# Optimization experiments

Measured on AMD Instinct MI355X. Metric: run time of the kernel, lower is better.

The kernel has to match this reference:

```python
import jax, jax.numpy as jnp
import numpy as np

N, E, IN, HID, Z, H = 10000, 320000, 128, 128, 64, 4


def setup_inputs() -> dict:
    key = jax.random.key(0)
    ks = jax.random.split(key, 24)
    s = 0.05
    inp = {
        "x": jax.random.normal(ks[0], (N, IN), jnp.float32),
        "edge_index": jax.random.randint(ks[1], (2, E), 0, N, jnp.int32),
        "eps": jax.random.normal(ks[2], (N, Z), jnp.float32),
        # GCNConv params
        "gcn_w": jax.random.normal(ks[3], (IN, HID), jnp.float32) * s,
        "gcn_b": jnp.zeros((HID,), jnp.float32),
        # GATConv params (heads=H, out=HID per head, concat=False)
        "gat_w": jax.random.normal(ks[4], (HID, H * HID), jnp.float32) * s,
        "gat_att_src": jax.random.normal(ks[5], (H, HID), jnp.float32) * s,
        "gat_att_dst": jax.random.normal(ks[6], (H, HID), jnp.float32) * s,
        "gat_b": jnp.zeros((HID,), jnp.float32),
        # encoder MLP
        "mlp_w1": jax.random.normal(ks[7], (HID, HID), jnp.float32) * s,
        "mlp_b1": jnp.zeros((HID,), jnp.float32),
        "mlp_w2": jax.random.normal(ks[8], (HID, HID), jnp.float32) * s,
        "mlp_b2": jnp.zeros((HID,), jnp.float32),
        "mu_w": jax.random.normal(ks[9], (HID, Z), jnp.float32) * s,
        "mu_b": jnp.zeros((Z,), jnp.float32),
        "lv_w": jax.random.normal(ks[10], (HID, Z), jnp.float32) * s,
        "lv_b": jnp.zeros((Z,), jnp.float32),
        # decoder
        "dec_w1": jax.random.normal(ks[11], (Z, HID), jnp.float32) * s,
        "dec_b1": jnp.zeros((HID,), jnp.float32),
        "dec_w2": jax.random.normal(ks[12], (HID, Z), jnp.float32) * s,
        "dec_b2": jnp.zeros((Z,), jnp.float32),
    }
    return inp


def _forward(x, eps, gcn_w, gcn_b, gat_w, gat_att_src, gat_att_dst, gat_b,
             mlp_w1, mlp_b1, mlp_w2, mlp_b2, mu_w, mu_b, lv_w, lv_b,
             dec_w1, dec_b1, dec_w2, dec_b2, src, dst):
    n = x.shape[0]
    # ---- GCNConv (symmetric norm, self loops already in src/dst) ----
    h = x @ gcn_w  # [N, HID]
    deg = jax.ops.segment_sum(jnp.ones_like(dst, jnp.float32), dst, num_segments=n)
    dinv = jnp.where(deg > 0, deg ** -0.5, 0.0)
    msg = h[src] * (dinv[src] * dinv[dst])[:, None]  # [E', HID]
    h = jax.nn.relu(jax.ops.segment_sum(msg, dst, num_segments=n) + gcn_b)
    # ---- GATConv (heads=H, concat=False -> mean over heads) ----
    g = (h @ gat_w).reshape(n, H, HID)  # [N,H,D]
    a_src = jnp.einsum("nhd,hd->nh", g, gat_att_src)  # [N,H]
    a_dst = jnp.einsum("nhd,hd->nh", g, gat_att_dst)
    e = jax.nn.leaky_relu(a_src[src] + a_dst[dst], 0.2)  # [E',H]
    emax = jax.ops.segment_max(e, dst, num_segments=n)
    ex = jnp.exp(e - emax[dst])
    den = jax.ops.segment_sum(ex, dst, num_segments=n)
    alpha = ex / den[dst]  # softmax over incoming edges
    agg = jax.ops.segment_sum(alpha[:, :, None] * g[src], dst, num_segments=n)
    h = jax.nn.relu(agg.mean(axis=1) + gat_b)  # [N,HID]
    # ---- MLP ----
    h = jax.nn.relu(h @ mlp_w1 + mlp_b1)
    h = jax.nn.relu(h @ mlp_w2 + mlp_b2)
    mu = h @ mu_w + mu_b
    logvar = h @ lv_w + lv_b
    # ---- reparameterize ----
    lv = jnp.clip(logvar, -10.0, 10.0)
    z = mu + eps * jnp.exp(0.5 * lv)
    # ---- decoder ----
    d = jax.nn.relu(z @ dec_w1 + dec_b1)
    d = d @ dec_w2 + dec_b2 + z
    logits = d @ d.T  # [N,N]
    return logits, mu, logvar


def reference(x, edge_index, eps, gcn_w, gcn_b, gat_w, gat_att_src, gat_att_dst,
              gat_b, mlp_w1, mlp_b1, mlp_w2, mlp_b2, mu_w, mu_b, lv_w, lv_b,
              dec_w1, dec_b1, dec_w2, dec_b2):
    n = x.shape[0]
    loop = jnp.arange(n, dtype=edge_index.dtype)
    src = jnp.concatenate([edge_index[0], loop])
    dst = jnp.concatenate([edge_index[1], loop])
    return _forward(x, eps, gcn_w, gcn_b, gat_w, gat_att_src, gat_att_dst,
                    gat_b, mlp_w1, mlp_b1, mlp_w2, mlp_b2, mu_w, mu_b,
                    lv_w, lv_b, dec_w1, dec_b1, dec_w2, dec_b2, src, dst)
```

## Files before the change

kernel.cpp:

```cpp
#include <hip/hip_runtime.h>
#include <hip/hip_bf16.h>

typedef unsigned short u16;
typedef unsigned int u32;

#define NN 10000
#define EE 320000

typedef __attribute__((ext_vector_type(8))) short short8;
typedef __attribute__((ext_vector_type(4))) float f32x4;

__device__ __forceinline__ u16 f2bfu(float f) {
    u32 x = __float_as_uint(f);
    x += 0x7FFFu + ((x >> 16) & 1u);
    return (u16)(x >> 16);
}
__device__ __forceinline__ float bfu2f(u16 u) { return __uint_as_float(((u32)u) << 16); }
__device__ __forceinline__ void ld4f(const float* p, float* o) {
    float4 v = *(const float4*)p; o[0] = v.x; o[1] = v.y; o[2] = v.z; o[3] = v.w;
}

__global__ void k_hist(const int* __restrict__ dst, int* __restrict__ cnt) {
    int e = blockIdx.x * 256 + threadIdx.x;
    if (e < EE) atomicAdd(&cnt[dst[e]], 1);
}

__global__ void k_scan(const int* __restrict__ cnt, int* __restrict__ rowptr,
                       float* __restrict__ dinv) {
    __shared__ int sh[1024];
    int t = threadIdx.x;
    int base = t * 10;
    int loc[10], cv[10];
    int s = 0;
    #pragma unroll
    for (int i = 0; i < 10; i++) {
        int idx = base + i;
        int v = (idx < NN) ? cnt[idx] : 0;
        cv[i] = v;
        loc[i] = s; s += v;
    }
    sh[t] = s;
    __syncthreads();
    for (int off = 1; off < 1024; off <<= 1) {
        int v = (t >= off) ? sh[t - off] : 0;
        __syncthreads();
        sh[t] += v;
        __syncthreads();
    }
    int ex = sh[t] - s;
    #pragma unroll
    for (int i = 0; i < 10; i++) {
        int idx = base + i;
        if (idx < NN) {
            rowptr[idx] = ex + loc[i];
            dinv[idx] = 1.f / sqrtf((float)(cv[i] + 1));
        }
    }
    if (t == 0) rowptr[NN] = EE;
}

__global__ void k_scatter(const int* __restrict__ src, const int* __restrict__ dst,
                          const int* __restrict__ rowptr, int* __restrict__ fill,
                          int* __restrict__ csr) {
    int e = blockIdx.x * 256 + threadIdx.x;
    if (e < EE) {
        int d = dst[e];
        int pos = rowptr[d] + atomicAdd(&fill[d], 1);
        csr[pos] = src[e];
    }
}

template <int K, int M, bool RELU, bool BIAS, bool OB16>
__global__ __launch_bounds__(256) void k_linear(const float* __restrict__ A, const float* __restrict__ W,
                                                const float* __restrict__ Bb, void* __restrict__ outv) {
    constexpr int MC = M / 64;
    int wid = (blockIdx.x * blockDim.x + threadIdx.x) >> 6;
    int lane = threadIdx.x & 63;
    int row0 = wid * 4;
    if (row0 >= NN) return;
    float acc[4][MC];
    #pragma unroll
    for (int i = 0; i < 4; i++)
        #pragma unroll
        for (int j = 0; j < MC; j++) acc[i][j] = 0.f;
    for (int k = 0; k < K; k += 4) {
        float a[4][4];
        #pragma unroll
        for (int i = 0; i < 4; i++) ld4f(A + (size_t)(row0 + i) * K + k, a[i]);
        #pragma unroll
        for (int kk = 0; kk < 4; kk++) {
            float wv[MC];
            #pragma unroll
            for (int j = 0; j < MC; j++) wv[j] = W[(size_t)(k + kk) * M + j * 64 + lane];
            #pragma unroll
            for (int i = 0; i < 4; i++)
                #pragma unroll
                for (int j = 0; j < MC; j++) acc[i][j] += a[i][kk] * wv[j];
        }
    }
    float* outf = (float*)outv;
    u16*   outb = (u16*)outv;
    #pragma unroll
    for (int i = 0; i < 4; i++) {
        int r = row0 + i;
        #pragma unroll
        for (int j = 0; j < MC; j++) {
            float v = acc[i][j];
            if constexpr (BIAS) v += Bb[j * 64 + lane];
            if constexpr (RELU) v = fmaxf(v, 0.f);
            if constexpr (OB16) outb[(size_t)r * M + j * 64 + lane] = f2bfu(v);
            else                outf[(size_t)r * M + j * 64 + lane] = v;
        }
    }
}

__global__ __launch_bounds__(256) void k_gcn_agg(const u16* __restrict__ h0, const int* __restrict__ rowptr,
                                                 const int* __restrict__ csr, const float* __restrict__ dinv,
                                                 const float* __restrict__ bias, float* __restrict__ h1) {
    int node = (blockIdx.x * blockDim.x + threadIdx.x) >> 6;
    int lane = threadIdx.x & 63;
    if (node >= NN) return;
    float di = dinv[node];
    u32 sv = *(const u32*)(h0 + (size_t)node * 128 + lane * 2);
    float acc0 = bfu2f((u16)(sv & 0xffffu)) * di * di;
    float acc1 = bfu2f((u16)(sv >> 16)) * di * di;
    int st = rowptr[node], en = rowptr[node + 1];
    for (int p = st; p < en; p++) {
        int s = csr[p];
        float w = dinv[s] * di;
        u32 gv = *(const u32*)(h0 + (size_t)s * 128 + lane * 2);
        acc0 += bfu2f((u16)(gv & 0xffffu)) * w;
        acc1 += bfu2f((u16)(gv >> 16)) * w;
    }
    acc0 = fmaxf(acc0 + bias[lane * 2], 0.f);
    acc1 = fmaxf(acc1 + bias[lane * 2 + 1], 0.f);
    float2 o; o.x = acc0; o.y = acc1;
    *(float2*)(h1 + (size_t)node * 128 + lane * 2) = o;
}

__global__ __launch_bounds__(256) void k_gat_linear(const float* __restrict__ A, const float* __restrict__ W,
                                                    const float* __restrict__ att_s, const float* __restrict__ att_d,
                                                    u16* __restrict__ gbf, float* __restrict__ a_src,
                                                    float* __restrict__ a_dst) {
    int wid = (blockIdx.x * blockDim.x + threadIdx.x) >> 6;
    int lane = threadIdx.x & 63;
    int row0 = wid * 4;
    if (row0 >= NN) return;
    float acc[4][8];
    #pragma unroll
    for (int i = 0; i < 4; i++)
        #pragma unroll
        for (int t = 0; t < 8; t++) acc[i][t] = 0.f;
    for (int k = 0; k < 128; k += 4) {
        float a[4][4];
        #pragma unroll
        for (int i = 0; i < 4; i++) ld4f(A + (size_t)(row0 + i) * 128 + k, a[i]);
        #pragma unroll
        for (int kk = 0; kk < 4; kk++) {
            float wv[8];
            ld4f(W + (size_t)(k + kk) * 512 + lane * 8, wv);
            ld4f(W + (size_t)(k + kk) * 512 + lane * 8 + 4, wv + 4);
            #pragma unroll
            for (int i = 0; i < 4; i++)
                #pragma unroll
                for (int t = 0; t < 8; t++) acc[i][t] += a[i][kk] * wv[t];
        }
    }
    float sv[8], dv[8];
    ld4f(att_s + lane * 8, sv); ld4f(att_s + lane * 8 + 4, sv + 4);
    ld4f(att_d + lane * 8, dv); ld4f(att_d + lane * 8 + 4, dv + 4);
    int head = lane >> 4;
    #pragma unroll
    for (int i = 0; i < 4; i++) {
        int r = row0 + i;
        short8 pk;
        #pragma unroll
        for (int t = 0; t < 8; t++) pk[t] = (short)f2bfu(acc[i][t]);
        *(short8*)(gbf + (size_t)r * 512 + lane * 8) = pk;
        float ps = 0.f, pd = 0.f;
        #pragma unroll
        for (int t = 0; t < 8; t++) { ps += acc[i][t] * sv[t]; pd += acc[i][t] * dv[t]; }
        #pragma unroll
        for (int off = 1; off < 16; off <<= 1) {
            ps += __shfl_xor(ps, off, 64);
            pd += __shfl_xor(pd, off, 64);
        }
        if ((lane & 15) == i) {
            a_src[r * 4 + head] = ps;
            a_dst[r * 4 + head] = pd;
        }
    }
}

__global__ __launch_bounds__(256) void k_gat_sa(const u16* __restrict__ gbf, const int* __restrict__ rowptr,
                                                const int* __restrict__ csr, const float* __restrict__ a_src,
                                                const float* __restrict__ a_dst, const float* __restrict__ bias,
                                                float* __restrict__ h2) {
    int node = (blockIdx.x * blockDim.x + threadIdx.x) >> 6;
    int lane = threadIdx.x & 63;
    if (node >= NN) return;
    int head = lane >> 4, l15 = lane & 15;
    float ad = a_dst[node * 4 + head];
    float es = a_src[node * 4 + head] + ad;
    es = es > 0.f ? es : 0.2f * es;
    float m = es;
    int st = rowptr[node], en = rowptr[node + 1];
    for (int p = st + l15; p < en; p += 16) {
        float e = a_src[csr[p] * 4 + head] + ad;
        e = e > 0.f ? e : 0.2f * e;
        m = fmaxf(m, e);
    }
    #pragma unroll
    for (int off = 1; off < 16; off <<= 1) m = fmaxf(m, __shfl_xor(m, off, 64));
    float w0 = __expf(es - m);
    float den = w0;
    float acc[8];
    short8 gs = *(const short8*)(gbf + (size_t)node * 512 + lane * 8);
    #pragma unroll
    for (int t = 0; t < 8; t++) acc[t] = w0 * bfu2f((u16)gs[t]);
    for (int p = st; p < en; p++) {
        int s = csr[p];
        float e = a_src[s * 4 + head] + ad;
        e = e > 0.f ? e : 0.2f * e;
        float w = __expf(e - m);
        den += w;
        short8 gv = *(const short8*)(gbf + (size_t)s * 512 + lane * 8);
        #pragma unroll
        for (int t = 0; t < 8; t++) acc[t] += w * bfu2f((u16)gv[t]);
    }
    float inv = 1.f / den;
    #pragma unroll
    for (int t = 0; t < 8; t++) acc[t] *= inv;
    #pragma unroll
    for (int t = 0; t < 8; t++) {
        acc[t] += __shfl_xor(acc[t], 16, 64);
        acc[t] += __shfl_xor(acc[t], 32, 64);
    }
    if (lane < 16) {
        int d0 = lane * 8;
        float o[8];
        #pragma unroll
        for (int t = 0; t < 8; t++) o[t] = fmaxf(acc[t] * 0.25f + bias[d0 + t], 0.f);
        float4 v0, v1;
        v0.x = o[0]; v0.y = o[1]; v0.z = o[2]; v0.w = o[3];
        v1.x = o[4]; v1.y = o[5]; v1.z = o[6]; v1.w = o[7];
        *(float4*)(h2 + (size_t)node * 128 + d0) = v0;
        *(float4*)(h2 + (size_t)node * 128 + d0 + 4) = v1;
    }
}

__global__ __launch_bounds__(256) void k_mlp(const float* __restrict__ A,
                                             const float* __restrict__ W1, const float* __restrict__ B1,
                                             const float* __restrict__ W2, const float* __restrict__ B2,
                                             const float* __restrict__ muW, const float* __restrict__ muB,
                                             const float* __restrict__ lvW, const float* __restrict__ lvB,
                                             const float* __restrict__ eps, float* __restrict__ mu_out,
                                             float* __restrict__ lv_out, float* __restrict__ z) {
    __shared__ float t[4][4][128];
    int wave = threadIdx.x >> 6;
    int lane = threadIdx.x & 63;
    int row0 = blockIdx.x * 16 + wave * 4;
    float acc[4][2];
    #pragma unroll
    for (int i = 0; i < 4; i++) { acc[i][0] = 0.f; acc[i][1] = 0.f; }
    for (int k = 0; k < 128; k += 4) {
        float a[4][4];
        #pragma unroll
        for (int i = 0; i < 4; i++) ld4f(A + (size_t)(row0 + i) * 128 + k, a[i]);
        #pragma unroll
        for (int kk = 0; kk < 4; kk++) {
            float w0 = W1[(size_t)(k + kk) * 128 + lane];
            float w1 = W1[(size_t)(k + kk) * 128 + 64 + lane];
            #pragma unroll
            for (int i = 0; i < 4; i++) { acc[i][0] += a[i][kk] * w0; acc[i][1] += a[i][kk] * w1; }
        }
    }
    #pragma unroll
    for (int i = 0; i < 4; i++) {
        t[wave][i][lane]      = fmaxf(acc[i][0] + B1[lane], 0.f);
        t[wave][i][64 + lane] = fmaxf(acc[i][1] + B1[64 + lane], 0.f);
    }
    float acc2[4][2];
    #pragma unroll
    for (int i = 0; i < 4; i++) { acc2[i][0] = 0.f; acc2[i][1] = 0.f; }
    for (int k = 0; k < 128; k += 4) {
        float a[4][4];
        #pragma unroll
        for (int i = 0; i < 4; i++) ld4f(&t[wave][i][k], a[i]);
        #pragma unroll
        for (int kk = 0; kk < 4; kk++) {
            float w0 = W2[(size_t)(k + kk) * 128 + lane];
            float w1 = W2[(size_t)(k + kk) * 128 + 64 + lane];
            #pragma unroll
            for (int i = 0; i < 4; i++) { acc2[i][0] += a[i][kk] * w0; acc2[i][1] += a[i][kk] * w1; }
        }
    }
    #pragma unroll
    for (int i = 0; i < 4; i++) {
        t[wave][i][lane]      = fmaxf(acc2[i][0] + B2[lane], 0.f);
        t[wave][i][64 + lane] = fmaxf(acc2[i][1] + B2[64 + lane], 0.f);
    }
    float am[4] = {0.f, 0.f, 0.f, 0.f};
    float av[4] = {0.f, 0.f, 0.f, 0.f};
    for (int k = 0; k < 128; k += 4) {
        float a[4][4];
        #pragma unroll
        for (int i = 0; i < 4; i++) ld4f(&t[wave][i][k], a[i]);
        #pragma unroll
        for (int kk = 0; kk < 4; kk++) {
            float wm = muW[(k + kk) * 64 + lane];
            float wl = lvW[(k + kk) * 64 + lane];
            #pragma unroll
            for (int i = 0; i < 4; i++) { am[i] += a[i][kk] * wm; av[i] += a[i][kk] * wl; }
        }
    }
    float bm = muB[lane], bl = lvB[lane];
    #pragma unroll
    for (int i = 0; i < 4; i++) {
        size_t idx = (size_t)(row0 + i) * 64 + lane;
        float mu = am[i] + bm;
        float lv = av[i] + bl;
        mu_out[idx] = mu;
        lv_out[idx] = lv;
        float c = fminf(fmaxf(lv, -10.f), 10.f);
        z[idx] = mu + eps[idx] * __expf(0.5f * c);
    }
}

__global__ __launch_bounds__(256) void k_dec(const float* __restrict__ z,
                                             const float* __restrict__ W1, const float* __restrict__ B1,
                                             const float* __restrict__ W2, const float* __restrict__ B2,
                                             u16* __restrict__ dbf) {
    __shared__ float t[4][4][128];
    int wave = threadIdx.x >> 6;
    int lane = threadIdx.x & 63;
    int row0 = blockIdx.x * 16 + wave * 4;
    float acc[4][2];
    #pragma unroll
    for (int i = 0; i < 4; i++) { acc[i][0] = 0.f; acc[i][1] = 0.f; }
    for (int k = 0; k < 64; k += 4) {
        float a[4][4];
        #pragma unroll
        for (int i = 0; i < 4; i++) ld4f(z + (size_t)(row0 + i) * 64 + k, a[i]);
        #pragma unroll
        for (int kk = 0; kk < 4; kk++) {
            float w0 = W1[(size_t)(k + kk) * 128 + lane];
            float w1 = W1[(size_t)(k + kk) * 128 + 64 + lane];
            #pragma unroll
            for (int i = 0; i < 4; i++) { acc[i][0] += a[i][kk] * w0; acc[i][1] += a[i][kk] * w1; }
        }
    }
    #pragma unroll
    for (int i = 0; i < 4; i++) {
        t[wave][i][lane]      = fmaxf(acc[i][0] + B1[lane], 0.f);
        t[wave][i][64 + lane] = fmaxf(acc[i][1] + B1[64 + lane], 0.f);
    }
    float acc2[4] = {0.f, 0.f, 0.f, 0.f};
    for (int k = 0; k < 128; k += 4) {
        float a[4][4];
        #pragma unroll
        for (int i = 0; i < 4; i++) ld4f(&t[wave][i][k], a[i]);
        #pragma unroll
        for (int kk = 0; kk < 4; kk++) {
            float wv = W2[(size_t)(k + kk) * 64 + lane];
            #pragma unroll
            for (int i = 0; i < 4; i++) acc2[i] += a[i][kk] * wv;
        }
    }
    float b = B2[lane];
    #pragma unroll
    for (int i = 0; i < 4; i++) {
        size_t idx = (size_t)(row0 + i) * 64 + lane;
        dbf[idx] = f2bfu(acc2[i] + b + z[idx]);
    }
}

__global__ __launch_bounds__(256) void k_logits(const u16* __restrict__ dbf, float* __restrict__ out) {
    __shared__ float tile[64][132];
    int tid = threadIdx.x;
    int wave = tid >> 6;
    int lane = tid & 63;
    int l15 = lane & 15, quad = lane >> 4;
    int rowhalf = wave >> 1;
    int i0 = blockIdx.y * 128 + rowhalf * 64;
    int j0 = blockIdx.x * 128 + (wave & 1) * 64;

    f32x4 acc[4][4];
    #pragma unroll
    for (int r = 0; r < 4; r++)
        #pragma unroll
        for (int c = 0; c < 4; c++) acc[r][c] = (f32x4){0.f, 0.f, 0.f, 0.f};

    #pragma unroll
    for (int ks = 0; ks < 64; ks += 32) {
        short8 a[4], b[4];
        #pragma unroll
        for (int r = 0; r < 4; r++) {
            int row = i0 + r * 16 + l15;
            if (row < NN) a[r] = *(const short8*)(dbf + (size_t)row * 64 + ks + quad * 8);
            else a[r] = (short8){0, 0, 0, 0, 0, 0, 0, 0};
        }
        #pragma unroll
        for (int c = 0; c < 4; c++) {
            int row = j0 + c * 16 + l15;
            if (row < NN) b[c] = *(const short8*)(dbf + (size_t)row * 64 + ks + quad * 8);
            else b[c] = (short8){0, 0, 0, 0, 0, 0, 0, 0};
        }
        #pragma unroll
        for (int r = 0; r < 4; r++)
            #pragma unroll
            for (int c = 0; c < 4; c++)
                acc[r][c] = __builtin_amdgcn_mfma_f32_16x16x32_bf16(a[r], b[c], acc[r][c], 0, 0, 0);
    }

    int lc0 = (wave & 1) * 64;
    #pragma unroll
    for (int chunk = 0; chunk < 2; chunk++) {
        if (rowhalf == chunk) {
            #pragma unroll
            for (int r = 0; r < 4; r++)
                #pragma unroll
                for (int c = 0; c < 4; c++)
                    #pragma unroll
                    for (int v = 0; v < 4; v++)
                        tile[r * 16 + quad * 4 + v][lc0 + c * 16 + l15] = acc[r][c][v];
        }
        __syncthreads();
        #pragma unroll
        for (int it = 0; it < 8; it++) {
            int idx = it * 256 + tid;
            int row = idx >> 5, ch = idx & 31;
            int rg = blockIdx.y * 128 + chunk * 64 + row;
            int cg = blockIdx.x * 128 + ch * 4;
            if (rg < NN && cg < NN) {
                f32x4 v = *(const f32x4*)&tile[row][ch * 4];
                __builtin_nontemporal_store(v, (f32x4*)(out + (size_t)rg * NN + cg));
            }
        }
        __syncthreads();
    }
}

extern "C" void kernel_launch(void* const* d_in, const int* in_sizes, int n_in,
                              void* d_out, int out_size, void* d_ws, size_t ws_size,
                              hipStream_t stream) {
    const float* x      = (const float*)d_in[0];
    const int*   ei     = (const int*)d_in[1];
    const float* eps    = (const float*)d_in[2];
    const float* gcn_w  = (const float*)d_in[3];
    const float* gcn_b  = (const float*)d_in[4];
    const float* gat_w  = (const float*)d_in[5];
    const float* att_s  = (const float*)d_in[6];
    const float* att_d  = (const float*)d_in[7];
    const float* gat_b  = (const float*)d_in[8];
    const float* mlp_w1 = (const float*)d_in[9];
    const float* mlp_b1 = (const float*)d_in[10];
    const float* mlp_w2 = (const float*)d_in[11];
    const float* mlp_b2 = (const float*)d_in[12];
    const float* mu_w   = (const float*)d_in[13];
    const float* mu_b   = (const float*)d_in[14];
    const float* lv_w   = (const float*)d_in[15];
    const float* lv_b   = (const float*)d_in[16];
    const float* dec_w1 = (const float*)d_in[17];
    const float* dec_b1 = (const float*)d_in[18];
    const float* dec_w2 = (const float*)d_in[19];
    const float* dec_b2 = (const float*)d_in[20];

    float* out    = (float*)d_out;
    float* out_mu = out + (size_t)NN * NN;
    float* out_lv = out_mu + (size_t)NN * 64;

    char* ws = (char*)d_ws;
    size_t off = 0;
    auto alloc = [&](size_t bytes) -> void* {
        void* p = ws + off;
        off += (bytes + 255) & ~(size_t)255;
        return p;
    };
    int*   cnt    = (int*)alloc(NN * 4);
    int*   fill   = (int*)alloc(NN * 4);
    int*   rowptr = (int*)alloc((NN + 1) * 4);
    int*   csr    = (int*)alloc(EE * 4);
    float* dinv   = (float*)alloc(NN * 4);
    float* a_src  = (float*)alloc(NN * 4 * 4);
    float* a_dst  = (float*)alloc(NN * 4 * 4);
    float* z      = (float*)alloc((size_t)NN * 64 * 4);
    float* h2     = (float*)alloc((size_t)NN * 128 * 4);
    float* bufA   = (float*)alloc((size_t)NN * 128 * 4);
    float* bufB   = (float*)alloc((size_t)NN * 128 * 4);
    float* bufC   = (float*)alloc((size_t)NN * 512 * 4);
    float* bufD   = (float*)alloc((size_t)NN * 64 * 2);

    u16*   h0bf = (u16*)bufA;
    float* h1   = bufB;
    u16*   gbf  = (u16*)bufC;
    u16*   dbf  = (u16*)bufD;

    const int* src = ei;
    const int* dst = ei + EE;

    hipMemsetAsync(cnt, 0, NN * 4, stream);
    hipMemsetAsync(fill, 0, NN * 4, stream);

    k_hist<<<(EE + 255) / 256, 256, 0, stream>>>(dst, cnt);
    k_scan<<<1, 1024, 0, stream>>>(cnt, rowptr, dinv);
    k_scatter<<<(EE + 255) / 256, 256, 0, stream>>>(src, dst, rowptr, fill, csr);

    k_linear<128, 128, false, false, true><<<625, 256, 0, stream>>>(x, gcn_w, nullptr, h0bf);
    k_gcn_agg<<<2500, 256, 0, stream>>>(h0bf, rowptr, csr, dinv, gcn_b, h1);

    k_gat_linear<<<625, 256, 0, stream>>>(h1, gat_w, att_s, att_d, gbf, a_src, a_dst);
    k_gat_sa<<<2500, 256, 0, stream>>>(gbf, rowptr, csr, a_src, a_dst, gat_b, h2);

    k_mlp<<<625, 256, 0, stream>>>(h2, mlp_w1, mlp_b1, mlp_w2, mlp_b2,
                                   mu_w, mu_b, lv_w, lv_b, eps, out_mu, out_lv, z);

    k_dec<<<625, 256, 0, stream>>>(z, dec_w1, dec_b1, dec_w2, dec_b2, dbf);

    dim3 lgrid((NN + 127) / 128, (NN + 127) / 128);
    k_logits<<<lgrid, 256, 0, stream>>>(dbf, out);
}
```

Measured before the change: 721.4 us.

## Use bf16 MFMA for GAT projection and online softmax in GAT aggregation

Replaces the FP32 scalar GAT linear kernel with a bf16 MFMA kernel, fed by a transposed bf16 copy of the weights and a bf16 GCN output. The attention logits are computed from the accumulators and the output is staged through shared memory for coalesced stores. The GAT aggregation drops its separate max pass over the edges and uses an online softmax with rescaling instead. This adds an extra weight-conversion kernel and rounds h1 to bf16, at some cost in precision.

```diff
diff --git a/kernel.cpp b/kernel.cpp
--- a/kernel.cpp
+++ b/kernel.cpp
@@ -67,6 +67,14 @@
         int d = dst[e];
         int pos = rowptr[d] + atomicAdd(&fill[d], 1);
         csr[pos] = src[e];
+    }
+}
+
+__global__ void k_wt(const float* __restrict__ w, u16* __restrict__ wt) {
+    int idx = blockIdx.x * 256 + threadIdx.x;
+    if (idx < 128 * 512) {
+        int k = idx >> 9, j = idx & 511;
+        wt[j * 128 + k] = f2bfu(w[idx]);
     }
 }
 
@@ -116,7 +124,7 @@
 
 __global__ __launch_bounds__(256) void k_gcn_agg(const u16* __restrict__ h0, const int* __restrict__ rowptr,
                                                  const int* __restrict__ csr, const float* __restrict__ dinv,
-                                                 const float* __restrict__ bias, float* __restrict__ h1) {
+                                                 const float* __restrict__ bias, u16* __restrict__ h1bf) {
     int node = (blockIdx.x * blockDim.x + threadIdx.x) >> 6;
     int lane = threadIdx.x & 63;
     if (node >= NN) return;
@@ -134,60 +142,104 @@
     }
     acc0 = fmaxf(acc0 + bias[lane * 2], 0.f);
     acc1 = fmaxf(acc1 + bias[lane * 2 + 1], 0.f);
-    float2 o; o.x = acc0; o.y = acc1;
-    *(float2*)(h1 + (size_t)node * 128 + lane * 2) = o;
-}
-
-__global__ __launch_bounds__(256) void k_gat_linear(const float* __restrict__ A, const float* __restrict__ W,
-                                                    const float* __restrict__ att_s, const float* __restrict__ att_d,
-                                                    u16* __restrict__ gbf, float* __restrict__ a_src,
-                                                    float* __restrict__ a_dst) {
-    int wid = (blockIdx.x * blockDim.x + threadIdx.x) >> 6;
-    int lane = threadIdx.x & 63;
-    int row0 = wid * 4;
-    if (row0 >= NN) return;
-    float acc[4][8];
-    #pragma unroll
-    for (int i = 0; i < 4; i++)
-        #pragma unroll
-        for (int t = 0; t < 8; t++) acc[i][t] = 0.f;
-    for (int k = 0; k < 128; k += 4) {
-        float a[4][4];
-        #pragma unroll
-        for (int i = 0; i < 4; i++) ld4f(A + (size_t)(row0 + i) * 128 + k, a[i]);
-        #pragma unroll
-        for (int kk = 0; kk < 4; kk++) {
-            float wv[8];
-            ld4f(W + (size_t)(k + kk) * 512 + lane * 8, wv);
-            ld4f(W + (size_t)(k + kk) * 512 + lane * 8 + 4, wv + 4);
-            #pragma unroll
-            for (int i = 0; i < 4; i++)
-                #pragma unroll
-                for (int t = 0; t < 8; t++) acc[i][t] += a[i][kk] * wv[t];
-        }
-    }
-    float sv[8], dv[8];
-    ld4f(att_s + lane * 8, sv); ld4f(att_s + lane * 8 + 4, sv + 4);
-    ld4f(att_d + lane * 8, dv); ld4f(att_d + lane * 8 + 4, dv + 4);
-    int head = lane >> 4;
-    #pragma unroll
-    for (int i = 0; i < 4; i++) {
-        int r = row0 + i;
-        short8 pk;
-        #pragma unroll
-        for (int t = 0; t < 8; t++) pk[t] = (short)f2bfu(acc[i][t]);
-        *(short8*)(gbf + (size_t)r * 512 + lane * 8) = pk;
-        float ps = 0.f, pd = 0.f;
-        #pragma unroll
-        for (int t = 0; t < 8; t++) { ps += acc[i][t] * sv[t]; pd += acc[i][t] * dv[t]; }
-        #pragma unroll
-        for (int off = 1; off < 16; off <<= 1) {
-            ps += __shfl_xor(ps, off, 64);
-            pd += __shfl_xor(pd, off, 64);
-        }
-        if ((lane & 15) == i) {
-            a_src[r * 4 + head] = ps;
-            a_dst[r * 4 + head] = pd;
+    u32 pack = (u32)f2bfu(acc0) | ((u32)f2bfu(acc1) << 16);
+    *(u32*)(h1bf + (size_t)node * 128 + lane * 2) = pack;
+}
+
+__global__ __launch_bounds__(256) void k_gat_mfma(const u16* __restrict__ h1bf, const u16* __restrict__ wt,
+                                                  const float* __restrict__ att_s, const float* __restrict__ att_d,
+                                                  u16* __restrict__ gbf, float* __restrict__ a_src,
+                                                  float* __restrict__ a_dst) {
+    __shared__ u16 gt[128][128];
+    __shared__ float ssrc[128][2], sdst[128][2];
+    int tid = threadIdx.x;
+    int wave = tid >> 6;
+    int lane = tid & 63;
+    int l15 = lane & 15, quad = lane >> 4;
+    int h = blockIdx.x;
+    int i0 = blockIdx.y * 128 + (wave >> 1) * 64;
+    int jh = (wave & 1) * 64;
+
+    f32x4 acc[4][4];
+    #pragma unroll
+    for (int r = 0; r < 4; r++)
+        #pragma unroll
+        for (int c = 0; c < 4; c++) acc[r][c] = (f32x4){0.f, 0.f, 0.f, 0.f};
+
+    #pragma unroll
+    for (int ks = 0; ks < 128; ks += 32) {
+        short8 a[4], b[4];
+        #pragma unroll
+        for (int r = 0; r < 4; r++) {
+            int row = i0 + r * 16 + l15;
+            if (row < NN) a[r] = *(const short8*)(h1bf + (size_t)row * 128 + ks + quad * 8);
+            else a[r] = (short8){0, 0, 0, 0, 0, 0, 0, 0};
+        }
+        #pragma unroll
+        for (int c = 0; c < 4; c++) {
+            int col = h * 128 + jh + c * 16 + l15;
+            b[c] = *(const short8*)(wt + (size_t)col * 128 + ks + quad * 8);
+        }
+        #pragma unroll
+        for (int r = 0; r < 4; r++)
+            #pragma unroll
+            for (int c = 0; c < 4; c++)
+                acc[r][c] = __builtin_amdgcn_mfma_f32_16x16x32_bf16(a[r], b[c], acc[r][c], 0, 0, 0);
+    }
+
+    float as_v[4], ad_v[4];
+    #pragma unroll
+    for (int c = 0; c < 4; c++) {
+        as_v[c] = att_s[h * 128 + jh + c * 16 + l15];
+        ad_v[c] = att_d[h * 128 + jh + c * 16 + l15];
+    }
+    #pragma unroll
+    for (int r = 0; r < 4; r++) {
+        #pragma unroll
+        for (int v = 0; v < 4; v++) {
+            float ps = 0.f, pd = 0.f;
+            #pragma unroll
+            for (int c = 0; c < 4; c++) {
+                float x = acc[r][c][v];
+                ps += x * as_v[c];
+                pd += x * ad_v[c];
+            }
+            #pragma unroll
+            for (int off = 1; off < 16; off <<= 1) {
+                ps += __shfl_xor(ps, off, 64);
+                pd += __shfl_xor(pd, off, 64);
+            }
+            if (l15 == 0) {
+                int lr = (wave >> 1) * 64 + r * 16 + quad * 4 + v;
+                ssrc[lr][wave & 1] = ps;
+                sdst[lr][wave & 1] = pd;
+            }
+        }
+    }
+    #pragma unroll
+    for (int r = 0; r < 4; r++)
+        #pragma unroll
+        for (int c = 0; c < 4; c++)
+            #pragma unroll
+            for (int v = 0; v < 4; v++)
+                gt[(wave >> 1) * 64 + r * 16 + quad * 4 + v][jh + c * 16 + l15] = f2bfu(acc[r][c][v]);
+    __syncthreads();
+
+    if (tid < 128) {
+        int row = blockIdx.y * 128 + tid;
+        if (row < NN) {
+            a_src[row * 4 + h] = ssrc[tid][0] + ssrc[tid][1];
+            a_dst[row * 4 + h] = sdst[tid][0] + sdst[tid][1];
+        }
+    }
+    #pragma unroll
+    for (int it = 0; it < 8; it++) {
+        int idx = it * 256 + tid;
+        int row = idx >> 4, ch = idx & 15;
+        int rg = blockIdx.y * 128 + row;
+        if (rg < NN) {
+            short8 v = *(const short8*)&gt[row][ch * 8];
+            *(short8*)(gbf + (size_t)rg * 512 + h * 128 + ch * 8) = v;
         }
     }
 }
@@ -199,29 +251,28 @@
     int node = (blockIdx.x * blockDim.x + threadIdx.x) >> 6;
     int lane = threadIdx.x & 63;
     if (node >= NN) return;
-    int head = lane >> 4, l15 = lane & 15;
+    int head = lane >> 4;
     float ad = a_dst[node * 4 + head];
     float es = a_src[node * 4 + head] + ad;
     es = es > 0.f ? es : 0.2f * es;
     float m = es;
-    int st = rowptr[node], en = rowptr[node + 1];
-    for (int p = st + l15; p < en; p += 16) {
-        float e = a_src[csr[p] * 4 + head] + ad;
-        e = e > 0.f ? e : 0.2f * e;
-        m = fmaxf(m, e);
-    }
-    #pragma unroll
-    for (int off = 1; off < 16; off <<= 1) m = fmaxf(m, __shfl_xor(m, off, 64));
-    float w0 = __expf(es - m);
-    float den = w0;
+    float den = 1.f;
     float acc[8];
     short8 gs = *(const short8*)(gbf + (size_t)node * 512 + lane * 8);
     #pragma unroll
-    for (int t = 0; t < 8; t++) acc[t] = w0 * bfu2f((u16)gs[t]);
+    for (int t = 0; t < 8; t++) acc[t] = bfu2f((u16)gs[t]);
+    int st = rowptr[node], en = rowptr[node + 1];
     for (int p = st; p < en; p++) {
         int s = csr[p];
         float e = a_src[s * 4 + head] + ad;
         e = e > 0.f ? e : 0.2f * e;
+        if (e > m) {
+            float sc = __expf(m - e);
+            den *= sc;
+            #pragma unroll
+            for (int t = 0; t < 8; t++) acc[t] *= sc;
+            m = e;
+        }
         float w = __expf(e - m);
         den += w;
         short8 gv = *(const short8*)(gbf + (size_t)s * 512 + lane * 8);
@@ -486,15 +537,11 @@
     float* a_dst  = (float*)alloc(NN * 4 * 4);
     float* z      = (float*)alloc((size_t)NN * 64 * 4);
     float* h2     = (float*)alloc((size_t)NN * 128 * 4);
-    float* bufA   = (float*)alloc((size_t)NN * 128 * 4);
-    float* bufB   = (float*)alloc((size_t)NN * 128 * 4);
-    float* bufC   = (float*)alloc((size_t)NN * 512 * 4);
-    float* bufD   = (float*)alloc((size_t)NN * 64 * 2);
-
-    u16*   h0bf = (u16*)bufA;
-    float* h1   = bufB;
-    u16*   gbf  = (u16*)bufC;
-    u16*   dbf  = (u16*)bufD;
+    u16*   wt     = (u16*)alloc(512 * 128 * 2);
+    u16*   h0bf   = (u16*)alloc((size_t)NN * 128 * 2);
+    u16*   h1bf   = (u16*)alloc((size_t)NN * 128 * 2);
+    u16*   gbf    = (u16*)alloc((size_t)NN * 512 * 2);
+    u16*   dbf    = (u16*)alloc((size_t)NN * 64 * 2);
 
     const int* src = ei;
     const int* dst = ei + EE;
@@ -502,14 +549,16 @@
     hipMemsetAsync(cnt, 0, NN * 4, stream);
     hipMemsetAsync(fill, 0, NN * 4, stream);
 
+    k_wt<<<(128 * 512 + 255) / 256, 256, 0, stream>>>(gat_w, wt);
     k_hist<<<(EE + 255) / 256, 256, 0, stream>>>(dst, cnt);
     k_scan<<<1, 1024, 0, stream>>>(cnt, rowptr, dinv);
     k_scatter<<<(EE + 255) / 256, 256, 0, stream>>>(src, dst, rowptr, fill, csr);
 
     k_linear<128, 128, false, false, true><<<625, 256, 0, stream>>>(x, gcn_w, nullptr, h0bf);
-    k_gcn_agg<<<2500, 256, 0, stream>>>(h0bf, rowptr, csr, dinv, gcn_b, h1);
-
-    k_gat_linear<<<625, 256, 0, stream>>>(h1, gat_w, att_s, att_d, gbf, a_src, a_dst);
+    k_gcn_agg<<<2500, 256, 0, stream>>>(h0bf, rowptr, csr, dinv, gcn_b, h1bf);
+
+    dim3 ggrid(4, (NN + 127) / 128);
+    k_gat_mfma<<<ggrid, 256, 0, stream>>>(h1bf, wt, att_s, att_d, gbf, a_src, a_dst);
     k_gat_sa<<<2500, 256, 0, stream>>>(gbf, rowptr, csr, a_src, a_dst, gat_b, h2);
 
     k_mlp<<<625, 256, 0, stream>>>(h2, mlp_w1, mlp_b1, mlp_w2, mlp_b2,
```

Measured after the change: 698.5 us. 1.03x faster.
